# Optimization experiments

Measured on AMD Instinct MI355X. Metric: run time of the kernel, lower is better.

The kernel has to match this reference:

```python
import jax, jax.numpy as jnp
import numpy as np

WS = 8          # window size
NH = 12         # heads
DM = 768        # d_model
HD = DM // NH   # head dim
SCALE = float(HD) ** 0.5


def _make_rel_coords():
    coords = np.stack(np.meshgrid(np.arange(WS), np.arange(WS), indexing='ij'))  # [2,ws,ws]
    coords = coords.reshape(2, -1)                                               # [2,L]
    rel = coords[:, :, None] - coords[:, None, :]                                # [2,L,L]
    rel = rel.transpose(1, 2, 0) + (WS - 1)                                      # [L,L,2]
    rel[:, :, 0] *= 2 * WS - 1
    return jnp.asarray(rel.sum(-1), dtype=jnp.int32)                             # [L,L]


def setup_inputs() -> dict:
    key = jax.random.key(0)
    ks = jax.random.split(key, 7)
    B, H, W = 8, 64, 64
    return {
        'x': jax.random.normal(ks[0], (B, DM, H, W), dtype=jnp.float32),
        'Wq': jax.random.normal(ks[1], (DM, DM), dtype=jnp.float32) * 0.02,
        'Wk': jax.random.normal(ks[2], (DM, DM), dtype=jnp.float32) * 0.02,
        'Wv': jax.random.normal(ks[3], (DM, DM), dtype=jnp.float32) * 0.02,
        'Wo_w': jax.random.normal(ks[4], (DM, DM), dtype=jnp.float32) * 0.02,
        'Wo_b': jax.random.normal(ks[5], (DM,), dtype=jnp.float32) * 0.02,
        'rel_pos_bias': jax.random.normal(ks[6], (NH, (2 * WS - 1) ** 2), dtype=jnp.float32) * 0.02,
        'rel_coords': _make_rel_coords(),
    }


def reference(x, Wq, Wk, Wv, Wo_w, Wo_b, rel_pos_bias, rel_coords):
    B, C, H, W = x.shape
    nh, nw = H // WS, W // WS
    L = WS * WS
    # b c (h wh) (w ww) -> b h w (wh ww) c
    xw = x.reshape(B, C, nh, WS, nw, WS).transpose(0, 2, 4, 3, 5, 1).reshape(B, nh, nw, L, C)

    def proj(Wm):  # Linear (no bias) then split heads: b h w l (n d) -> b h w n l d
        y = jnp.einsum('bhwlc,oc->bhwlo', xw, Wm)
        return y.reshape(B, nh, nw, L, NH, HD).transpose(0, 1, 2, 4, 3, 5)

    q, k, v = proj(Wq), proj(Wk), proj(Wv)
    bias = rel_pos_bias[:, rel_coords]                               # [NH, L, L]
    attn = jnp.einsum('bhwnld,bhwnmd->bhwnlm', q, k) / SCALE + bias
    p = jax.nn.softmax(attn, axis=-1)
    o = jnp.einsum('bhwnlm,bhwnmd->bhwnld', p, v)                    # [B,nh,nw,NH,L,HD]
    # b h w n (wh ww) d -> b (n d) (h wh) (w ww)
    o = o.reshape(B, nh, nw, NH, WS, WS, HD)
    o = o.transpose(0, 3, 6, 1, 4, 2, 5).reshape(B, C, H, W)
    # 1x1 conv with bias
    return jnp.einsum('bchw,oc->bohw', o, Wo_w) + Wo_b[None, :, None, None]
```

## Files before the change

### kernel.cpp

```cpp
#include <hip/hip_runtime.h>


#define DM      768
#define NHEADS  12
#define HD      64
#define LTOK    64
#define NWIN    512

typedef __attribute__((ext_vector_type(8))) short bf16x8;
typedef __attribute__((ext_vector_type(4))) float f32x4;

__device__ __forceinline__ unsigned short f2bf(float f) {
    union { float f; unsigned u; } v; v.f = f;
    unsigned r = v.u + 0x7FFFu + ((v.u >> 16) & 1u);
    return (unsigned short)(r >> 16);
}
__device__ __forceinline__ float bf2f(unsigned short h) {
    union { unsigned u; float f; } v; v.u = ((unsigned)h) << 16;
    return v.f;
}
__device__ __forceinline__ void gl_lds16(const void* g, void* l) {
    __builtin_amdgcn_global_load_lds(
        (const __attribute__((address_space(1))) void*)g,
        (__attribute__((address_space(3))) void*)l, 16, 0, 0);
}

__global__ __launch_bounds__(256)
void xprep_kernel(const float* __restrict__ x,
                  unsigned short* __restrict__ Xhi,
                  unsigned short* __restrict__ Xlo)
{
    __shared__ float lds[32][33];
    const int tid = threadIdx.x;
    const int px0 = blockIdx.x * 32;
    const int c0  = blockIdx.y * 32;
    const int b   = blockIdx.z;
    {
        const int cc = tid >> 3, w4 = tid & 7;
        const float4 v = *(const float4*)(
            x + ((size_t)(b * DM + c0 + cc)) * 4096 + px0 + w4 * 4);
        lds[cc][w4*4+0] = v.x; lds[cc][w4*4+1] = v.y;
        lds[cc][w4*4+2] = v.z; lds[cc][w4*4+3] = v.w;
    }
    __syncthreads();
    const int tpx = tid >> 3, cg = tid & 7;
    const int p = px0 + tpx, h = p >> 6, w = p & 63;
    const int t = (((b << 6) | ((h >> 3) << 3) | (w >> 3)) << 6)
                | ((h & 7) << 3) | (w & 7);
    const size_t dst = (size_t)t * DM + c0 + cg * 4;
    const float f0 = lds[cg*4+0][tpx], f1 = lds[cg*4+1][tpx],
                f2 = lds[cg*4+2][tpx], f3 = lds[cg*4+3][tpx];
    ushort4 hv, lv;
    hv.x = f2bf(f0); lv.x = f2bf(f0 - bf2f(hv.x));
    hv.y = f2bf(f1); lv.y = f2bf(f1 - bf2f(hv.y));
    hv.z = f2bf(f2); lv.z = f2bf(f2 - bf2f(hv.z));
    hv.w = f2bf(f3); lv.w = f2bf(f3 - bf2f(hv.w));
    *(ushort4*)(Xhi + dst) = hv;
    *(ushort4*)(Xlo + dst) = lv;
}

__global__ __launch_bounds__(256)
void fsplit_kernel(const float* __restrict__ src,
                   unsigned short* __restrict__ hi,
                   unsigned short* __restrict__ lo, int n)
{
    const int i = (blockIdx.x * 256 + threadIdx.x) * 4;
    if (i >= n) return;
    const float4 v = *(const float4*)(src + i);
    ushort4 hv, lv;
    hv.x = f2bf(v.x); lv.x = f2bf(v.x - bf2f(hv.x));
    hv.y = f2bf(v.y); lv.y = f2bf(v.y - bf2f(hv.y));
    hv.z = f2bf(v.z); lv.z = f2bf(v.z - bf2f(hv.z));
    hv.w = f2bf(v.w); lv.w = f2bf(v.w - bf2f(hv.w));
    *(ushort4*)(hi + i) = hv;
    *(ushort4*)(lo + i) = lv;
}

#define GEMM_PROLOGUE(AHIP, ALOP, BHIP, BLOP)                                  \
    __shared__ f32x4 smem4[2048];                      \
    char* const smem = (char*)smem4;                                           \
    const int tid  = threadIdx.x;                                              \
    const int lane = tid & 63, wv = tid >> 6;                                  \
    const int wr = wv >> 1, wc = wv & 1;                                       \
    const int nt = blockIdx.x;                                                 \
    const int m0 = blockIdx.y * 128;                                           \
    const int n0 = nt * 128;                                                   \
    const int rql = lane >> 2;                                                 \
    const int gsw = (lane & 3) ^ ((lane >> 3) & 3);                            \
    const char* gb0 = (const char*)(AHIP) + (size_t)m0 * 1536;                 \
    const char* gb1 = (const char*)(ALOP) + (size_t)m0 * 1536;                 \
    const char* gb2 = (const char*)(BHIP) + (size_t)n0 * 1536;                 \
    const char* gb3 = (const char*)(BLOP) + (size_t)n0 * 1536;                 \
    const int l15 = lane & 15, kg = lane >> 4;                                 \
    const int kgp = kg ^ ((l15 >> 1) & 3);                                     \
    int aoff[4], boff[4];                                                      \
    _Pragma("unroll")                                                          \
    for (int f = 0; f < 4; ++f) {                                              \
        aoff[f] = (wr * 64 + f * 16 + l15) * 64 + kgp * 16;                    \
        boff[f] = (wc * 64 + f * 16 + l15) * 64 + kgp * 16;                    \
    }                                                                          \
    f32x4 acc[4][4];                                                           \
    _Pragma("unroll")                                                          \
    for (int i = 0; i < 4; ++i)                                                \
        _Pragma("unroll")                                                      \
        for (int j = 0; j < 4; ++j) acc[i][j] = (f32x4){0.f, 0.f, 0.f, 0.f};   \
    _Pragma("unroll 1")                                                        \
    for (int kt = 0; kt < DM; kt += 32) {                                      \
        const size_t kb = (size_t)kt * 2;                                      \
        _Pragma("unroll")                                                      \
        for (int q = 0; q < 8; ++q) {                                          \
            const int tt = q >> 1;                                             \
            const int s  = wv * 2 + (q & 1);                                   \
            const int r  = s * 16 + rql;                                       \
            const char* srcp = (tt == 0 ? gb0 : tt == 1 ? gb1 :                \
                                tt == 2 ? gb2 : gb3)                           \
                               + (size_t)r * 1536 + kb + gsw * 16;             \
            gl_lds16(srcp, smem + tt * 8192 + s * 1024);                       \
        }                                                                      \
        __syncthreads();                                                       \
        bf16x8 ah[4], al[4], bh[4], bl[4];                                     \
        _Pragma("unroll")                                                      \
        for (int f = 0; f < 4; ++f) {                                          \
            ah[f] = *(const bf16x8*)(smem +     0 + aoff[f]);                  \
            al[f] = *(const bf16x8*)(smem +  8192 + aoff[f]);                  \
            bh[f] = *(const bf16x8*)(smem + 16384 + boff[f]);                  \
            bl[f] = *(const bf16x8*)(smem + 24576 + boff[f]);                  \
        }                                                                      \
        _Pragma("unroll")                                                      \
        for (int mi = 0; mi < 4; ++mi)                                         \
            _Pragma("unroll")                                                  \
            for (int ni = 0; ni < 4; ++ni) {                                   \
                acc[mi][ni] = __builtin_amdgcn_mfma_f32_16x16x32_bf16(         \
                    ah[mi], bh[ni], acc[mi][ni], 0, 0, 0);                     \
                acc[mi][ni] = __builtin_amdgcn_mfma_f32_16x16x32_bf16(         \
                    ah[mi], bl[ni], acc[mi][ni], 0, 0, 0);                     \
                acc[mi][ni] = __builtin_amdgcn_mfma_f32_16x16x32_bf16(         \
                    al[mi], bh[ni], acc[mi][ni], 0, 0, 0);                     \
            }                                                                  \
        __syncthreads();                                                       \
    }

__global__ __launch_bounds__(256, 2)
void qkv_mfma_kernel(const unsigned short* __restrict__ Xhi,
                     const unsigned short* __restrict__ Xlo,
                     const unsigned short* __restrict__ Whi,
                     const unsigned short* __restrict__ Wlo,
                     float* __restrict__ Q, float* __restrict__ K,
                     float* __restrict__ V)
{
    GEMM_PROLOGUE(Xhi, Xlo, Whi, Wlo)

    const int mat = nt / 6, c6 = nt % 6;
    float* __restrict__ Out = (mat == 0) ? Q : (mat == 1) ? K : V;
    const float scale = (mat == 0) ? 0.125f : 1.0f;
    const int head = c6 * 2 + wc;
#pragma unroll
    for (int mi = 0; mi < 4; ++mi) {
#pragma unroll
        for (int qq = 0; qq < 4; ++qq) {
            const int m   = m0 + wr * 64 + mi * 16 + kg * 4 + qq;
            const int win = m >> 6, tok = m & 63;
            float* rowp = Out + (size_t)win * 49152 + head * 4096 + tok * 64;
#pragma unroll
            for (int ni = 0; ni < 4; ++ni)
                rowp[ni * 16 + l15] = acc[mi][ni][qq] * scale;
        }
    }
}

__global__ __launch_bounds__(256, 2)
void outproj_mfma_kernel(const unsigned short* __restrict__ Ohi,
                         const unsigned short* __restrict__ Olo,
                         const unsigned short* __restrict__ Wohi,
                         const unsigned short* __restrict__ Wolo,
                         const float* __restrict__ Wb,
                         float* __restrict__ out)
{
    GEMM_PROLOGUE(Ohi, Olo, Wohi, Wolo)

    float bsv[4];
    int   ocol[4];
#pragma unroll
    for (int ni = 0; ni < 4; ++ni) {
        ocol[ni] = n0 + wc * 64 + ni * 16 + l15;
        bsv[ni]  = Wb[ocol[ni]];
    }
#pragma unroll
    for (int mi = 0; mi < 4; ++mi) {
#pragma unroll
        for (int qq = 0; qq < 4; ++qq) {
            const int m    = m0 + wr * 64 + mi * 16 + kg * 4 + qq;
            const int win  = m >> 6, tl = m & 63;
            const int bimg = win >> 6, wh = (win >> 3) & 7, ww = win & 7;
            const int h = wh * 8 + (tl >> 3), w = ww * 8 + (tl & 7);
            float* pix = out + (size_t)bimg * DM * 4096 + (size_t)h * 64 + w;
#pragma unroll
            for (int ni = 0; ni < 4; ++ni)
                pix[(size_t)ocol[ni] * 4096] = acc[mi][ni][qq] + bsv[ni];
        }
    }
}

__global__ __launch_bounds__(256)
void attn_kernel(const float* __restrict__ Q,
                 const float* __restrict__ K,
                 const float* __restrict__ V,
                 const float* __restrict__ rpb,
                 const int*   __restrict__ coords,
                 unsigned short* __restrict__ Obhi,
                 unsigned short* __restrict__ Oblo)
{
    const int win  = blockIdx.x;
    const int head = blockIdx.y;
    const int tid  = threadIdx.x;
    const int tx = tid & 15, ty = tid >> 4;

    __shared__ float qs[64][65];
    __shared__ float ks[64][65];
    __shared__ float vs[64][65];

    const int base = (win * NHEADS + head) * (LTOK * HD);

#pragma unroll
    for (int r = 0; r < 4; ++r) {
        const int f = tid + r * 256;
        const int e = f * 4;
        const int l = e >> 6, d = e & 63;
        float4 t;
        t = *(const float4*)(Q + base + e);
        qs[l][d] = t.x; qs[l][d+1] = t.y; qs[l][d+2] = t.z; qs[l][d+3] = t.w;
        t = *(const float4*)(K + base + e);
        ks[l][d] = t.x; ks[l][d+1] = t.y; ks[l][d+2] = t.z; ks[l][d+3] = t.w;
        t = *(const float4*)(V + base + e);
        vs[l][d] = t.x; vs[l][d+1] = t.y; vs[l][d+2] = t.z; vs[l][d+3] = t.w;
    }
    __syncthreads();

    float acc[4][4];
#pragma unroll
    for (int i = 0; i < 4; ++i)
#pragma unroll
        for (int j = 0; j < 4; ++j) acc[i][j] = 0.0f;

    for (int d = 0; d < HD; ++d) {
        float a[4], bb[4];
#pragma unroll
        for (int i = 0; i < 4; ++i) a[i]  = qs[ty*4+i][d];
#pragma unroll
        for (int j = 0; j < 4; ++j) bb[j] = ks[tx*4+j][d];
#pragma unroll
        for (int i = 0; i < 4; ++i)
#pragma unroll
            for (int j = 0; j < 4; ++j) acc[i][j] += a[i] * bb[j];
    }

#pragma unroll
    for (int i = 0; i < 4; ++i) {
        const int l = ty*4 + i;
#pragma unroll
        for (int j = 0; j < 4; ++j)
            acc[i][j] += rpb[head * 225 + coords[l * 64 + tx*4 + j]];
    }

    float inv[4];
#pragma unroll
    for (int i = 0; i < 4; ++i) {
        float mx = fmaxf(fmaxf(acc[i][0], acc[i][1]),
                         fmaxf(acc[i][2], acc[i][3]));
#pragma unroll
        for (int off = 1; off < 16; off <<= 1)
            mx = fmaxf(mx, __shfl_xor(mx, off));
        float s = 0.0f;
#pragma unroll
        for (int j = 0; j < 4; ++j) {
            acc[i][j] = expf(acc[i][j] - mx);
            s += acc[i][j];
        }
#pragma unroll
        for (int off = 1; off < 16; off <<= 1)
            s += __shfl_xor(s, off);
        inv[i] = 1.0f / s;
    }

    __syncthreads();
#pragma unroll
    for (int i = 0; i < 4; ++i)
#pragma unroll
        for (int j = 0; j < 4; ++j)
            qs[ty*4+i][tx*4+j] = acc[i][j] * inv[i];
    __syncthreads();

    float o[4][4];
#pragma unroll
    for (int i = 0; i < 4; ++i)
#pragma unroll
        for (int j = 0; j < 4; ++j) o[i][j] = 0.0f;

    for (int m = 0; m < LTOK; ++m) {
        float a[4], bb[4];
#pragma unroll
        for (int i = 0; i < 4; ++i) a[i]  = qs[ty*4+i][m];
#pragma unroll
        for (int j = 0; j < 4; ++j) bb[j] = vs[m][tx*4+j];
#pragma unroll
        for (int i = 0; i < 4; ++i)
#pragma unroll
            for (int j = 0; j < 4; ++j) o[i][j] += a[i] * bb[j];
    }

    unsigned short* dh = Obhi + (size_t)(win * LTOK) * DM + head * HD + tx * 4;
    unsigned short* dl = Oblo + (size_t)(win * LTOK) * DM + head * HD + tx * 4;
#pragma unroll
    for (int i = 0; i < 4; ++i) {
        const int l = ty*4 + i;
        ushort4 hv, lv;
        hv.x = f2bf(o[i][0]); lv.x = f2bf(o[i][0] - bf2f(hv.x));
        hv.y = f2bf(o[i][1]); lv.y = f2bf(o[i][1] - bf2f(hv.y));
        hv.z = f2bf(o[i][2]); lv.z = f2bf(o[i][2] - bf2f(hv.z));
        hv.w = f2bf(o[i][3]); lv.w = f2bf(o[i][3] - bf2f(hv.w));
        *(ushort4*)(dh + (size_t)l * DM) = hv;
        *(ushort4*)(dl + (size_t)l * DM) = lv;
    }
}

extern "C" void kernel_launch(void* const* d_in, const int* in_sizes, int n_in,
                              void* d_out, int out_size, void* d_ws, size_t ws_size,
                              hipStream_t stream)
{
    const float* x   = (const float*)d_in[0];
    const float* Wq  = (const float*)d_in[1];
    const float* Wk  = (const float*)d_in[2];
    const float* Wv  = (const float*)d_in[3];
    const float* Wo  = (const float*)d_in[4];
    const float* Wb  = (const float*)d_in[5];
    const float* rpb = (const float*)d_in[6];
    const int*   rc  = (const int*)d_in[7];
    float* out = (float*)d_out;

    char* ws = (char*)d_ws;
    unsigned short* Xhi = (unsigned short*)ws;
    unsigned short* Xlo = (unsigned short*)(ws + 50331648);
    float* Qb = (float*)(ws + 100663296);
    float* Kb = Qb + 25165824;
    float* Vb = Kb + 25165824;

    unsigned short* Whi = (unsigned short*)d_out;
    unsigned short* Wlo = Whi + 1769472;
    unsigned short* Wohi = (unsigned short*)Qb;
    unsigned short* Wolo = Wohi + 589824;

    unsigned short* Obhi = Xhi;
    unsigned short* Oblo = Xlo;

    xprep_kernel<<<dim3(128, 24, 8), 256, 0, stream>>>(x, Xhi, Xlo);
    fsplit_kernel<<<576, 256, 0, stream>>>(Wq, Whi,           Wlo,           589824);
    fsplit_kernel<<<576, 256, 0, stream>>>(Wk, Whi +  589824, Wlo +  589824, 589824);
    fsplit_kernel<<<576, 256, 0, stream>>>(Wv, Whi + 1179648, Wlo + 1179648, 589824);

    qkv_mfma_kernel<<<dim3(18, 256), 256, 0, stream>>>(Xhi, Xlo, Whi, Wlo,
                                                       Qb, Kb, Vb);
    attn_kernel<<<dim3(NWIN, NHEADS), 256, 0, stream>>>(Qb, Kb, Vb, rpb, rc,
                                                        Obhi, Oblo);
    fsplit_kernel<<<576, 256, 0, stream>>>(Wo, Wohi, Wolo, 589824);
    outproj_mfma_kernel<<<dim3(6, 256), 256, 0, stream>>>(Obhi, Oblo,
                                                          Wohi, Wolo, Wb, out);
}
```

Before: 899.8 us.

## Move window attention to split-bf16 MFMA with bf16 hi/lo Q/K/V-transposed storage

The scalar fp32 attention kernel becomes an MFMA kernel with one wave per head, using 3-term bf16 hi/lo splitting for QK^T and PV to keep close-to-fp32 accuracy. The QKV GEMM epilogue now writes Q and K as bf16 hi/lo pairs and V transposed, so attention can load MFMA fragments straight from global memory. Softmax probabilities are staged in swizzled LDS. The transposed V stores are strided scalar writes and may be less coalesced in the GEMM epilogue.

```diff
diff --git a/kernel.cpp b/kernel.cpp
--- a/kernel.cpp
+++ b/kernel.cpp
@@ -145,25 +145,56 @@
                      const unsigned short* __restrict__ Xlo,
                      const unsigned short* __restrict__ Whi,
                      const unsigned short* __restrict__ Wlo,
-                     float* __restrict__ Q, float* __restrict__ K,
-                     float* __restrict__ V)
+                     unsigned short* __restrict__ Qhi,
+                     unsigned short* __restrict__ Qlo,
+                     unsigned short* __restrict__ Khi,
+                     unsigned short* __restrict__ Klo,
+                     unsigned short* __restrict__ Vthi,
+                     unsigned short* __restrict__ Vtlo)
 {
     GEMM_PROLOGUE(Xhi, Xlo, Whi, Wlo)
 
     const int mat = nt / 6, c6 = nt % 6;
-    float* __restrict__ Out = (mat == 0) ? Q : (mat == 1) ? K : V;
-    const float scale = (mat == 0) ? 0.125f : 1.0f;
     const int head = c6 * 2 + wc;
-#pragma unroll
-    for (int mi = 0; mi < 4; ++mi) {
-#pragma unroll
-        for (int qq = 0; qq < 4; ++qq) {
-            const int m   = m0 + wr * 64 + mi * 16 + kg * 4 + qq;
-            const int win = m >> 6, tok = m & 63;
-            float* rowp = Out + (size_t)win * 49152 + head * 4096 + tok * 64;
-#pragma unroll
-            for (int ni = 0; ni < 4; ++ni)
-                rowp[ni * 16 + l15] = acc[mi][ni][qq] * scale;
+    if (mat < 2) {
+        unsigned short* __restrict__ Hi = (mat == 0) ? Qhi : Khi;
+        unsigned short* __restrict__ Lo = (mat == 0) ? Qlo : Klo;
+        const float scale = (mat == 0) ? 0.125f : 1.0f;
+#pragma unroll
+        for (int mi = 0; mi < 4; ++mi) {
+#pragma unroll
+            for (int qq = 0; qq < 4; ++qq) {
+                const int m   = m0 + wr * 64 + mi * 16 + kg * 4 + qq;
+                const int win = m >> 6, tok = m & 63;
+                const size_t rb = ((size_t)(win * NHEADS + head) * 64 + tok) * 64;
+#pragma unroll
+                for (int ni = 0; ni < 4; ++ni) {
+                    const int d = ni * 16 + l15;
+                    const float f = acc[mi][ni][qq] * scale;
+                    const unsigned short h = f2bf(f);
+                    Hi[rb + d] = h;
+                    Lo[rb + d] = f2bf(f - bf2f(h));
+                }
+            }
+        }
+    } else {
+#pragma unroll
+        for (int mi = 0; mi < 4; ++mi) {
+#pragma unroll
+            for (int qq = 0; qq < 4; ++qq) {
+                const int m   = m0 + wr * 64 + mi * 16 + kg * 4 + qq;
+                const int win = m >> 6, tok = m & 63;
+                const size_t hb = (size_t)(win * NHEADS + head) * 4096;
+#pragma unroll
+                for (int ni = 0; ni < 4; ++ni) {
+                    const int d = ni * 16 + l15;
+                    const float f = acc[mi][ni][qq];
+                    const unsigned short h = f2bf(f);
+                    const size_t a = hb + (size_t)d * 64 + tok;
+                    Vthi[a] = h;
+                    Vtlo[a] = f2bf(f - bf2f(h));
+                }
+            }
         }
     }
 }
@@ -201,125 +232,143 @@
     }
 }
 
-__global__ __launch_bounds__(256)
-void attn_kernel(const float* __restrict__ Q,
-                 const float* __restrict__ K,
-                 const float* __restrict__ V,
-                 const float* __restrict__ rpb,
-                 const int*   __restrict__ coords,
-                 unsigned short* __restrict__ Obhi,
-                 unsigned short* __restrict__ Oblo)
-{
+__global__ __launch_bounds__(256, 2)
+void attn_mfma_kernel(const unsigned short* __restrict__ Qhi,
+                      const unsigned short* __restrict__ Qlo,
+                      const unsigned short* __restrict__ Khi,
+                      const unsigned short* __restrict__ Klo,
+                      const unsigned short* __restrict__ Vthi,
+                      const unsigned short* __restrict__ Vtlo,
+                      const float* __restrict__ rpb,
+                      const int*   __restrict__ coords,
+                      unsigned short* __restrict__ Obhi,
+                      unsigned short* __restrict__ Oblo)
+{
+    __shared__ f32x4 plds4[4096];
+    char* const pldsb = (char*)plds4;
+
+    const int tid  = threadIdx.x;
+    const int lane = tid & 63, wvi = tid >> 6;
+    const int l15 = lane & 15, kg = lane >> 4;
     const int win  = blockIdx.x;
-    const int head = blockIdx.y;
-    const int tid  = threadIdx.x;
-    const int tx = tid & 15, ty = tid >> 4;
-
-    __shared__ float qs[64][65];
-    __shared__ float ks[64][65];
-    __shared__ float vs[64][65];
-
-    const int base = (win * NHEADS + head) * (LTOK * HD);
-
-#pragma unroll
-    for (int r = 0; r < 4; ++r) {
-        const int f = tid + r * 256;
-        const int e = f * 4;
-        const int l = e >> 6, d = e & 63;
-        float4 t;
-        t = *(const float4*)(Q + base + e);
-        qs[l][d] = t.x; qs[l][d+1] = t.y; qs[l][d+2] = t.z; qs[l][d+3] = t.w;
-        t = *(const float4*)(K + base + e);
-        ks[l][d] = t.x; ks[l][d+1] = t.y; ks[l][d+2] = t.z; ks[l][d+3] = t.w;
-        t = *(const float4*)(V + base + e);
-        vs[l][d] = t.x; vs[l][d+1] = t.y; vs[l][d+2] = t.z; vs[l][d+3] = t.w;
-    }
-    __syncthreads();
-
-    float acc[4][4];
+    const int head = blockIdx.y * 4 + wvi;
+    const size_t base = (size_t)(win * NHEADS + head) * 4096;
+    char* const pw = pldsb + wvi * 16384;
+
+    bf16x8 qh[4][2], ql[4][2], kh[4][2], kl[4][2];
 #pragma unroll
     for (int i = 0; i < 4; ++i)
 #pragma unroll
-        for (int j = 0; j < 4; ++j) acc[i][j] = 0.0f;
-
-    for (int d = 0; d < HD; ++d) {
-        float a[4], bb[4];
-#pragma unroll
-        for (int i = 0; i < 4; ++i) a[i]  = qs[ty*4+i][d];
-#pragma unroll
-        for (int j = 0; j < 4; ++j) bb[j] = ks[tx*4+j][d];
-#pragma unroll
-        for (int i = 0; i < 4; ++i)
-#pragma unroll
-            for (int j = 0; j < 4; ++j) acc[i][j] += a[i] * bb[j];
-    }
-
-#pragma unroll
-    for (int i = 0; i < 4; ++i) {
-        const int l = ty*4 + i;
-#pragma unroll
-        for (int j = 0; j < 4; ++j)
-            acc[i][j] += rpb[head * 225 + coords[l * 64 + tx*4 + j]];
-    }
-
-    float inv[4];
-#pragma unroll
-    for (int i = 0; i < 4; ++i) {
-        float mx = fmaxf(fmaxf(acc[i][0], acc[i][1]),
-                         fmaxf(acc[i][2], acc[i][3]));
-#pragma unroll
-        for (int off = 1; off < 16; off <<= 1)
-            mx = fmaxf(mx, __shfl_xor(mx, off));
-        float s = 0.0f;
-#pragma unroll
-        for (int j = 0; j < 4; ++j) {
-            acc[i][j] = expf(acc[i][j] - mx);
-            s += acc[i][j];
-        }
-#pragma unroll
-        for (int off = 1; off < 16; off <<= 1)
-            s += __shfl_xor(s, off);
-        inv[i] = 1.0f / s;
-    }
-
-    __syncthreads();
-#pragma unroll
-    for (int i = 0; i < 4; ++i)
-#pragma unroll
-        for (int j = 0; j < 4; ++j)
-            qs[ty*4+i][tx*4+j] = acc[i][j] * inv[i];
-    __syncthreads();
-
-    float o[4][4];
-#pragma unroll
-    for (int i = 0; i < 4; ++i)
-#pragma unroll
-        for (int j = 0; j < 4; ++j) o[i][j] = 0.0f;
-
-    for (int m = 0; m < LTOK; ++m) {
-        float a[4], bb[4];
-#pragma unroll
-        for (int i = 0; i < 4; ++i) a[i]  = qs[ty*4+i][m];
-#pragma unroll
-        for (int j = 0; j < 4; ++j) bb[j] = vs[m][tx*4+j];
-#pragma unroll
-        for (int i = 0; i < 4; ++i)
-#pragma unroll
-            for (int j = 0; j < 4; ++j) o[i][j] += a[i] * bb[j];
-    }
-
-    unsigned short* dh = Obhi + (size_t)(win * LTOK) * DM + head * HD + tx * 4;
-    unsigned short* dl = Oblo + (size_t)(win * LTOK) * DM + head * HD + tx * 4;
-#pragma unroll
-    for (int i = 0; i < 4; ++i) {
-        const int l = ty*4 + i;
-        ushort4 hv, lv;
-        hv.x = f2bf(o[i][0]); lv.x = f2bf(o[i][0] - bf2f(hv.x));
-        hv.y = f2bf(o[i][1]); lv.y = f2bf(o[i][1] - bf2f(hv.y));
-        hv.z = f2bf(o[i][2]); lv.z = f2bf(o[i][2] - bf2f(hv.z));
-        hv.w = f2bf(o[i][3]); lv.w = f2bf(o[i][3] - bf2f(hv.w));
-        *(ushort4*)(dh + (size_t)l * DM) = hv;
-        *(ushort4*)(dl + (size_t)l * DM) = lv;
+        for (int ks = 0; ks < 2; ++ks) {
+            const size_t o = base + (size_t)(i * 16 + l15) * 64 + ks * 32 + kg * 8;
+            qh[i][ks] = *(const bf16x8*)(Qhi + o);
+            ql[i][ks] = *(const bf16x8*)(Qlo + o);
+            kh[i][ks] = *(const bf16x8*)(Khi + o);
+            kl[i][ks] = *(const bf16x8*)(Klo + o);
+        }
+
+    f32x4 s[4][4];
+#pragma unroll
+    for (int li = 0; li < 4; ++li)
+#pragma unroll
+        for (int mi = 0; mi < 4; ++mi) s[li][mi] = (f32x4){0.f, 0.f, 0.f, 0.f};
+#pragma unroll
+    for (int li = 0; li < 4; ++li)
+#pragma unroll
+        for (int mi = 0; mi < 4; ++mi)
+#pragma unroll
+            for (int ks = 0; ks < 2; ++ks) {
+                s[li][mi] = __builtin_amdgcn_mfma_f32_16x16x32_bf16(
+                    qh[li][ks], kh[mi][ks], s[li][mi], 0, 0, 0);
+                s[li][mi] = __builtin_amdgcn_mfma_f32_16x16x32_bf16(
+                    qh[li][ks], kl[mi][ks], s[li][mi], 0, 0, 0);
+                s[li][mi] = __builtin_amdgcn_mfma_f32_16x16x32_bf16(
+                    ql[li][ks], kh[mi][ks], s[li][mi], 0, 0, 0);
+            }
+
+    const float* rpbh = rpb + head * 225;
+#pragma unroll
+    for (int li = 0; li < 4; ++li) {
+#pragma unroll
+        for (int q = 0; q < 4; ++q) {
+            const int r = li * 16 + kg * 4 + q;
+            float pv[4];
+#pragma unroll
+            for (int mi = 0; mi < 4; ++mi)
+                pv[mi] = s[li][mi][q] + rpbh[coords[r * 64 + mi * 16 + l15]];
+            float mx = fmaxf(fmaxf(pv[0], pv[1]), fmaxf(pv[2], pv[3]));
+#pragma unroll
+            for (int off = 1; off < 16; off <<= 1)
+                mx = fmaxf(mx, __shfl_xor(mx, off));
+            float sum = 0.0f;
+#pragma unroll
+            for (int mi = 0; mi < 4; ++mi) {
+                pv[mi] = expf(pv[mi] - mx);
+                sum += pv[mi];
+            }
+#pragma unroll
+            for (int off = 1; off < 16; off <<= 1)
+                sum += __shfl_xor(sum, off);
+            const float inv = 1.0f / sum;
+#pragma unroll
+            for (int mi = 0; mi < 4; ++mi) {
+                const float p = pv[mi] * inv;
+                const unsigned short h = f2bf(p);
+                const unsigned short l = f2bf(p - bf2f(h));
+                const int byt = (r * 128 + (mi * 16 + l15) * 2) ^ ((r & 7) << 4);
+                *(unsigned short*)(pw + byt)        = h;
+                *(unsigned short*)(pw + 8192 + byt) = l;
+            }
+        }
+    }
+
+    bf16x8 vh[4][2], vl[4][2];
+#pragma unroll
+    for (int di = 0; di < 4; ++di)
+#pragma unroll
+        for (int ks = 0; ks < 2; ++ks) {
+            const size_t o = base + (size_t)(di * 16 + l15) * 64 + ks * 32 + kg * 8;
+            vh[di][ks] = *(const bf16x8*)(Vthi + o);
+            vl[di][ks] = *(const bf16x8*)(Vtlo + o);
+        }
+
+#pragma unroll
+    for (int li = 0; li < 4; ++li) {
+        bf16x8 ph[2], pl[2];
+#pragma unroll
+        for (int ks = 0; ks < 2; ++ks) {
+            const int row = li * 16 + l15;
+            const int byt = (row * 128 + ks * 64 + kg * 16) ^ ((row & 7) << 4);
+            ph[ks] = *(const bf16x8*)(pw + byt);
+            pl[ks] = *(const bf16x8*)(pw + 8192 + byt);
+        }
+        f32x4 oacc[4];
+#pragma unroll
+        for (int di = 0; di < 4; ++di) oacc[di] = (f32x4){0.f, 0.f, 0.f, 0.f};
+#pragma unroll
+        for (int di = 0; di < 4; ++di)
+#pragma unroll
+            for (int ks = 0; ks < 2; ++ks) {
+                oacc[di] = __builtin_amdgcn_mfma_f32_16x16x32_bf16(
+                    ph[ks], vh[di][ks], oacc[di], 0, 0, 0);
+                oacc[di] = __builtin_amdgcn_mfma_f32_16x16x32_bf16(
+                    ph[ks], vl[di][ks], oacc[di], 0, 0, 0);
+                oacc[di] = __builtin_amdgcn_mfma_f32_16x16x32_bf16(
+                    pl[ks], vh[di][ks], oacc[di], 0, 0, 0);
+            }
+#pragma unroll
+        for (int q = 0; q < 4; ++q) {
+            const int ltok = li * 16 + kg * 4 + q;
+            const size_t rb = (size_t)(win * LTOK + ltok) * DM + head * HD;
+#pragma unroll
+            for (int di = 0; di < 4; ++di) {
+                const int d = di * 16 + l15;
+                const float f = oacc[di][q];
+                const unsigned short h = f2bf(f);
+                Obhi[rb + d] = h;
+                Oblo[rb + d] = f2bf(f - bf2f(h));
+            }
+        }
     }
 }
 
@@ -340,13 +389,16 @@
     char* ws = (char*)d_ws;
     unsigned short* Xhi = (unsigned short*)ws;
     unsigned short* Xlo = (unsigned short*)(ws + 50331648);
-    float* Qb = (float*)(ws + 100663296);
-    float* Kb = Qb + 25165824;
-    float* Vb = Kb + 25165824;
+    unsigned short* Qhi  = (unsigned short*)(ws + 100663296);
+    unsigned short* Qlo  = Qhi  + 25165824;
+    unsigned short* Khi  = Qlo  + 25165824;
+    unsigned short* Klo  = Khi  + 25165824;
+    unsigned short* Vthi = Klo  + 25165824;
+    unsigned short* Vtlo = Vthi + 25165824;
 
     unsigned short* Whi = (unsigned short*)d_out;
     unsigned short* Wlo = Whi + 1769472;
-    unsigned short* Wohi = (unsigned short*)Qb;
+    unsigned short* Wohi = Qhi;
     unsigned short* Wolo = Wohi + 589824;
 
     unsigned short* Obhi = Xhi;
@@ -357,10 +409,10 @@
     fsplit_kernel<<<576, 256, 0, stream>>>(Wk, Whi +  589824, Wlo +  589824, 589824);
     fsplit_kernel<<<576, 256, 0, stream>>>(Wv, Whi + 1179648, Wlo + 1179648, 589824);
 
-    qkv_mfma_kernel<<<dim3(18, 256), 256, 0, stream>>>(Xhi, Xlo, Whi, Wlo,
-                                                       Qb, Kb, Vb);
-    attn_kernel<<<dim3(NWIN, NHEADS), 256, 0, stream>>>(Qb, Kb, Vb, rpb, rc,
-                                                        Obhi, Oblo);
+    qkv_mfma_kernel<<<dim3(18, 256), 256, 0, stream>>>(
+        Xhi, Xlo, Whi, Wlo, Qhi, Qlo, Khi, Klo, Vthi, Vtlo);
+    attn_mfma_kernel<<<dim3(NWIN, 3), 256, 0, stream>>>(
+        Qhi, Qlo, Khi, Klo, Vthi, Vtlo, rpb, rc, Obhi, Oblo);
     fsplit_kernel<<<576, 256, 0, stream>>>(Wo, Wohi, Wolo, 589824);
     outproj_mfma_kernel<<<dim3(6, 256), 256, 0, stream>>>(Obhi, Oblo,
                                                           Wohi, Wolo, Wb, out);
```

Measured after the change: 881.8 us. 2.0% less time.
